# Performance work log

Hardware: AMD Instinct MI355X
Metric: run time of the kernel (lower is better)

The kernel has to match this reference:

```python
import jax, jax.numpy as jnp
import numpy as np

B, S, H = 2, 2048, 2048
NH, HD = 32, 64          # num heads, head dim (H = NH*HD)
ROT = 16                 # rotary_ndims = int(HD * rope_pct=0.25)
THETA = 10000.0
MAXPOS = 4096
NEG_INF = -1e30


def _rope_cache():
    inv_freq = 1.0 / (THETA ** (jnp.arange(0, ROT, 2, dtype=jnp.float32) / ROT))
    t = jnp.arange(MAXPOS, dtype=jnp.float32)
    freqs = jnp.outer(t, inv_freq)              # [MAXPOS, ROT/2]
    emb = jnp.concatenate([freqs, freqs], -1)   # [MAXPOS, ROT]
    return jnp.cos(emb), jnp.sin(emb)


def _rotate_half(x):
    x1, x2 = jnp.split(x, 2, axis=-1)
    return jnp.concatenate([-x2, x1], axis=-1)


def setup_inputs() -> dict:
    key = jax.random.key(0)
    k1, k2, k3 = jax.random.split(key, 3)
    hidden_states = jax.random.normal(k1, (B, S, H), dtype=jnp.float32)
    qkv_w = jax.random.normal(k2, (3 * H, H), dtype=jnp.float32) * 0.02
    o_w = jax.random.normal(k3, (H, H), dtype=jnp.float32) * 0.02
    position_ids = (jnp.arange(B * S).reshape(B, S) % MAXPOS).astype(jnp.int32)
    return {"hidden_states": hidden_states, "qkv_w": qkv_w, "o_w": o_w,
            "position_ids": position_ids}


def reference(hidden_states, qkv_w, o_w, position_ids):
    b, s, _ = hidden_states.shape
    # fused QKV projection (Linear, no bias): x @ W^T
    qkv = hidden_states @ qkv_w.T                      # [b, s, 3H]
    q, k, v = jnp.split(qkv, 3, axis=-1)
    # (b, s, nh*hd) -> (b, nh, s, hd)
    q = q.reshape(b, s, NH, HD).transpose(0, 2, 1, 3)
    k = k.reshape(b, s, NH, HD).transpose(0, 2, 1, 3)
    v = v.reshape(b, s, NH, HD).transpose(0, 2, 1, 3)

    # partial RoPE on first ROT dims
    cos, sin = _rope_cache()
    cos = cos[position_ids][:, None]                   # [b, 1, s, ROT]
    sin = sin[position_ids][:, None]
    q_rot, q_pass = q[..., :ROT], q[..., ROT:]
    k_rot, k_pass = k[..., :ROT], k[..., ROT:]
    q_rot = q_rot * cos + _rotate_half(q_rot) * sin
    k_rot = k_rot * cos + _rotate_half(k_rot) * sin
    q = jnp.concatenate([q_rot, q_pass], axis=-1)
    k = jnp.concatenate([k_rot, k_pass], axis=-1)

    # causal scaled-dot-product attention (prefill branch, layer_past=None)
    scale = 1.0 / jnp.sqrt(jnp.float32(HD))
    scores = jnp.einsum('bhqd,bhkd->bhqk', q, k) * scale
    causal = jnp.tril(jnp.ones((s, s), dtype=bool))
    scores = jnp.where(causal, scores, NEG_INF)
    weights = jax.nn.softmax(scores.astype(jnp.float32), axis=-1).astype(q.dtype)
    attn = jnp.einsum('bhqk,bhkd->bhqd', weights, v)   # [b, nh, s, hd]

    attn = attn.transpose(0, 2, 1, 3).reshape(b, s, NH * HD)
    return attn @ o_w.T
```

## Files before the change

kernel.cpp:

```cpp
#include <hip/hip_runtime.h>
#include <hip/hip_bf16.h>
#include <math.h>

#define B_   2
#define S_   2048
#define H_   2048
#define NH_  32
#define HD_  64

typedef __bf16 bf16_t;
typedef bf16_t bf16x8 __attribute__((ext_vector_type(8)));
typedef float  f32x4  __attribute__((ext_vector_type(4)));
typedef unsigned short u16x8 __attribute__((ext_vector_type(8)));

__device__ __forceinline__ float bf2f(unsigned short u) {
  unsigned int x = ((unsigned int)u) << 16;
  return __builtin_bit_cast(float, x);
}
__device__ __forceinline__ unsigned short f2bf(float f) {
  unsigned int u = __builtin_bit_cast(unsigned int, f);
  u += 0x7FFFu + ((u >> 16) & 1u);
  return (unsigned short)(u >> 16);
}

__device__ __forceinline__ void gload16(const void* g, void* l) {
  __builtin_amdgcn_global_load_lds((const __attribute__((address_space(1))) void*)g,
                                   (__attribute__((address_space(3))) void*)l, 16, 0, 0);
}

__global__ void cast_kernel(const float* __restrict__ in, unsigned short* __restrict__ out, int n4) {
  int stride = gridDim.x * blockDim.x;
  for (int i = blockIdx.x * blockDim.x + threadIdx.x; i < n4; i += stride) {
    float4 v = reinterpret_cast<const float4*>(in)[i];
    ushort4 o;
    o.x = f2bf(v.x); o.y = f2bf(v.y); o.z = f2bf(v.z); o.w = f2bf(v.w);
    reinterpret_cast<ushort4*>(out)[i] = o;
  }
}

template<int EPI>
__global__ __launch_bounds__(256) void gemm_bt(
    const unsigned short* __restrict__ A, const unsigned short* __restrict__ Bt,
    float* __restrict__ outF,
    unsigned short* __restrict__ qb, unsigned short* __restrict__ kb, unsigned short* __restrict__ vb,
    int M, int N, int K)
{
  __shared__ unsigned short As[128 * 64];
  __shared__ unsigned short Bs[128 * 64];
  const int tid  = threadIdx.x;
  const int lane = tid & 63;
  const int wave = tid >> 6;
  const int lo = lane & 15, hi = lane >> 4;
  const int wr = wave >> 1, wc = wave & 1;
  const int m0 = blockIdx.x * 128;
  const int n0 = blockIdx.y * 128;

  const unsigned short* asrc[4];
  const unsigned short* bsrc[4];
  unsigned short* adst[4];
  unsigned short* bdst[4];
#pragma unroll
  for (int i = 0; i < 4; ++i) {
    int idx = i * 256 + tid;
    int r  = idx >> 3;
    int cb = (idx & 7) * 16;
    int cs = cb ^ ((r & 7) << 4);
    asrc[i] = A  + (size_t)(m0 + r) * K + (cs >> 1);
    bsrc[i] = Bt + (size_t)(n0 + r) * K + (cs >> 1);
    adst[i] = &As[idx * 8];
    bdst[i] = &Bs[idx * 8];
  }

  f32x4 zero = {0.f, 0.f, 0.f, 0.f};
  f32x4 acc[4][4];
#pragma unroll
  for (int i = 0; i < 4; ++i)
#pragma unroll
    for (int j = 0; j < 4; ++j) acc[i][j] = zero;

  for (int k0 = 0; k0 < K; k0 += 64) {
    __syncthreads();
#pragma unroll
    for (int i = 0; i < 4; ++i) gload16(asrc[i] + k0, adst[i]);
#pragma unroll
    for (int i = 0; i < 4; ++i) gload16(bsrc[i] + k0, bdst[i]);
    __syncthreads();
#pragma unroll
    for (int kk = 0; kk < 2; ++kk) {
      bf16x8 af[4], bfm[4];
#pragma unroll
      for (int i = 0; i < 4; ++i) {
        int ra = wr * 64 + i * 16 + lo;
        af[i] = *reinterpret_cast<const bf16x8*>(
            (const char*)As + ra * 128 + ((kk * 64 + hi * 16) ^ ((ra & 7) << 4)));
        int rb = wc * 64 + i * 16 + lo;
        bfm[i] = *reinterpret_cast<const bf16x8*>(
            (const char*)Bs + rb * 128 + ((kk * 64 + hi * 16) ^ ((rb & 7) << 4)));
      }
#pragma unroll
      for (int i = 0; i < 4; ++i)
#pragma unroll
        for (int j = 0; j < 4; ++j)
          acc[i][j] = __builtin_amdgcn_mfma_f32_16x16x32_bf16(af[i], bfm[j], acc[i][j], 0, 0, 0);
    }
  }

#pragma unroll
  for (int i = 0; i < 4; ++i) {
#pragma unroll
    for (int j = 0; j < 4; ++j) {
#pragma unroll
      for (int r = 0; r < 4; ++r) {
        int row = m0 + wr * 64 + i * 16 + hi * 4 + r;
        int col = n0 + wc * 64 + j * 16 + lo;
        float v = acc[i][j][r];
        if (EPI == 0) {
          int sec = col >> 11;
          int hh  = (col >> 6) & 31;
          int d   = col & 63;
          int b   = row >> 11;
          int s   = row & 2047;
          unsigned short bv = f2bf(v);
          size_t off = ((size_t)(b * NH_ + hh) * S_ + s) * HD_ + d;
          if (sec == 0)      qb[off] = bv;
          else if (sec == 1) kb[off] = bv;
          else               vb[off] = bv;
        } else {
          outF[(size_t)row * N + col] = v;
        }
      }
    }
  }
}

__global__ __launch_bounds__(256) void vtrans_kernel(const unsigned short* __restrict__ vb,
                                                     unsigned short* __restrict__ vt) {
  __shared__ unsigned short T[64 * 64];
  const int s0 = blockIdx.x * 64;
  const int bh = blockIdx.y;
  const unsigned short* src = vb + (size_t)bh * S_ * HD_ + (size_t)s0 * HD_;
  unsigned short* dst = vt + (size_t)bh * HD_ * S_ + s0;
  const int t = threadIdx.x;
#pragma unroll
  for (int pass = 0; pass < 2; ++pass) {
    int r  = pass * 32 + (t >> 3);
    int c8 = t & 7;
    u16x8 v = *reinterpret_cast<const u16x8*>(src + r * HD_ + c8 * 8);
    *reinterpret_cast<u16x8*>((char*)T + r * 128 + ((c8 * 16) ^ ((r & 7) << 4))) = v;
  }
  __syncthreads();
#pragma unroll
  for (int pass = 0; pass < 2; ++pass) {
    int d  = pass * 32 + (t >> 3);
    int sc = t & 7;
    u16x8 v;
#pragma unroll
    for (int i = 0; i < 8; ++i) {
      int s = sc * 8 + i;
      v[i] = *(const unsigned short*)((const char*)T + s * 128 + ((2 * d) ^ ((s & 7) << 4)));
    }
    *reinterpret_cast<u16x8*>(dst + (size_t)d * S_ + sc * 8) = v;
  }
}

__global__ void rope_kernel(unsigned short* __restrict__ qb, unsigned short* __restrict__ kb,
                            const int* __restrict__ pos) {
  int idx = blockIdx.x * blockDim.x + threadIdx.x;
  if (idx >= B_ * NH_ * S_) return;
  int s  = idx & (S_ - 1);
  int bh = idx >> 11;
  int b  = bh >> 5;
  float p = (float)pos[b * S_ + s];
  const float invf[8] = {1.0f, 0.31622776601683794f, 0.1f, 0.031622776601683791f,
                         0.01f, 0.0031622776601683794f, 0.001f, 0.00031622776601683794f};
  unsigned short* q = qb + (size_t)idx * HD_;
  unsigned short* k = kb + (size_t)idx * HD_;
#pragma unroll
  for (int i = 0; i < 8; ++i) {
    float ang = p * invf[i];
    float sn, c;
    sincosf(ang, &sn, &c);
    float q1 = bf2f(q[i]), q2 = bf2f(q[i + 8]);
    q[i]     = f2bf(q1 * c - q2 * sn);
    q[i + 8] = f2bf(q2 * c + q1 * sn);
    float k1 = bf2f(k[i]), k2 = bf2f(k[i + 8]);
    k[i]     = f2bf(k1 * c - k2 * sn);
    k[i + 8] = f2bf(k2 * c + k1 * sn);
  }
}

__global__ __launch_bounds__(256, 2) void attn_fwd(
    const unsigned short* __restrict__ qb, const unsigned short* __restrict__ kb,
    const unsigned short* __restrict__ vt, unsigned short* __restrict__ ob)
{
  __shared__ unsigned short Ks[2][64 * 64];
  __shared__ unsigned short Vs[2][64 * 64];
  __shared__ unsigned short Ps[4][2][32 * 64];
  const int bid  = blockIdx.x;
  const int j    = bid >> 6;
  const int bh   = bid & 63;
  const int tid  = threadIdx.x;
  const int lane = tid & 63;
  const int wave = tid >> 6;
  const int lo = lane & 15, hi = lane >> 4;
  const int b = bh >> 5, h = bh & 31;
  const unsigned short* Qg = qb + (size_t)bh * S_ * HD_;
  const unsigned short* Kg = kb + (size_t)bh * S_ * HD_;
  const unsigned short* Vg = vt + (size_t)bh * HD_ * S_;

  const int qrow0[2] = {j * 128 + wave * 32, (15 - j) * 128 + wave * 32};

  const float qscale = 0.125f * 1.4426950408889634f;
  bf16x8 aq[2][2][2];
#pragma unroll
  for (int t = 0; t < 2; ++t)
#pragma unroll
    for (int rf = 0; rf < 2; ++rf)
#pragma unroll
      for (int kk = 0; kk < 2; ++kk) {
        bf16x8 tt = *reinterpret_cast<const bf16x8*>(
            Qg + (size_t)(qrow0[t] + rf * 16 + lo) * HD_ + kk * 32 + hi * 8);
#pragma unroll
        for (int e = 0; e < 8; ++e) aq[t][rf][kk][e] = (bf16_t)((float)tt[e] * qscale);
      }

  f32x4 zero = {0.f, 0.f, 0.f, 0.f};
  float m_s[2][2][4], l_s[2][2][4];
  f32x4 o_acc[2][2][4];
#pragma unroll
  for (int t = 0; t < 2; ++t)
#pragma unroll
    for (int rf = 0; rf < 2; ++rf)
#pragma unroll
      for (int r = 0; r < 4; ++r) {
        m_s[t][rf][r] = -1e30f; l_s[t][rf][r] = 0.f;
        o_acc[t][rf][r] = zero;
      }

  auto stage = [&](int kt, int buf) {
#pragma unroll
    for (int i = 0; i < 2; ++i) {
      int idx = i * 256 + tid;
      int r   = idx >> 3;
      int cs  = ((idx & 7) * 16) ^ ((r & 7) << 4);
      gload16(Kg + (size_t)(kt * 64 + r) * HD_ + (cs >> 1), &Ks[buf][idx * 8]);
      gload16(Vg + (size_t)r * S_ + kt * 64 + (cs >> 1), &Vs[buf][idx * 8]);
    }
  };

  const int nkt = 2 * (15 - j) + 2;
  stage(0, 0);

  for (int kt = 0; kt < nkt; ++kt) {
    const int cur = kt & 1;
    if (kt + 1 < nkt) {
      stage(kt + 1, cur ^ 1);
      asm volatile("s_waitcnt vmcnt(4)" ::: "memory");
    } else {
      asm volatile("s_waitcnt vmcnt(0)" ::: "memory");
    }
    __builtin_amdgcn_s_barrier();
    __builtin_amdgcn_sched_barrier(0);

    bf16x8 bk[4][2];
#pragma unroll
    for (int ct = 0; ct < 4; ++ct)
#pragma unroll
      for (int kk = 0; kk < 2; ++kk) {
        int row = ct * 16 + lo;
        bk[ct][kk] = *reinterpret_cast<const bf16x8*>(
            (const char*)&Ks[cur][0] + row * 128 + ((kk * 64 + hi * 16) ^ ((row & 7) << 4)));
      }

#pragma unroll
    for (int t = 0; t < 2; ++t) {
      if (kt * 64 <= qrow0[t] + 31) {
        f32x4 sc[2][4];
        __builtin_amdgcn_s_setprio(1);
#pragma unroll
        for (int rf = 0; rf < 2; ++rf)
#pragma unroll
          for (int ct = 0; ct < 4; ++ct) {
            f32x4 a = zero;
            a = __builtin_amdgcn_mfma_f32_16x16x32_bf16(aq[t][rf][0], bk[ct][0], a, 0, 0, 0);
            a = __builtin_amdgcn_mfma_f32_16x16x32_bf16(aq[t][rf][1], bk[ct][1], a, 0, 0, 0);
            sc[rf][ct] = a;
          }
        __builtin_amdgcn_s_setprio(0);

        if (kt * 64 + 63 > qrow0[t]) {
#pragma unroll
          for (int rf = 0; rf < 2; ++rf)
#pragma unroll
            for (int ct = 0; ct < 4; ++ct)
#pragma unroll
              for (int rr = 0; rr < 4; ++rr) {
                int qrow = qrow0[t] + rf * 16 + hi * 4 + rr;
                int kcol = kt * 64 + ct * 16 + lo;
                if (kcol > qrow) sc[rf][ct][rr] = -1e30f;
              }
        }

#pragma unroll
        for (int rf = 0; rf < 2; ++rf) {
#pragma unroll
          for (int rr = 0; rr < 4; ++rr) {
            float tm = fmaxf(fmaxf(sc[rf][0][rr], sc[rf][1][rr]),
                             fmaxf(sc[rf][2][rr], sc[rf][3][rr]));
            tm = fmaxf(tm, __shfl_xor(tm, 1));
            tm = fmaxf(tm, __shfl_xor(tm, 2));
            tm = fmaxf(tm, __shfl_xor(tm, 4));
            tm = fmaxf(tm, __shfl_xor(tm, 8));
            float mn = fmaxf(m_s[t][rf][rr], tm);
            float corr = exp2f(m_s[t][rf][rr] - mn);
            m_s[t][rf][rr] = mn;
            float rs = 0.f;
#pragma unroll
            for (int ct = 0; ct < 4; ++ct) {
              float e = exp2f(sc[rf][ct][rr] - mn);
              sc[rf][ct][rr] = e;
              rs += e;
            }
            rs += __shfl_xor(rs, 1);
            rs += __shfl_xor(rs, 2);
            rs += __shfl_xor(rs, 4);
            rs += __shfl_xor(rs, 8);
            l_s[t][rf][rr] = l_s[t][rf][rr] * corr + rs;
#pragma unroll
            for (int dt = 0; dt < 4; ++dt) o_acc[t][rf][dt][rr] *= corr;
          }
        }

        char* pw = (char*)&Ps[wave][t][0];
#pragma unroll
        for (int rf = 0; rf < 2; ++rf)
#pragma unroll
          for (int ct = 0; ct < 4; ++ct)
#pragma unroll
            for (int rr = 0; rr < 4; ++rr) {
              int row = rf * 16 + hi * 4 + rr;
              *(unsigned short*)(pw + row * 128 + ((2 * (ct * 16 + lo)) ^ ((row & 7) << 4))) =
                  f2bf(sc[rf][ct][rr]);
            }
      }
    }

    bf16x8 bv[4][2];
#pragma unroll
    for (int dt = 0; dt < 4; ++dt)
#pragma unroll
      for (int kk = 0; kk < 2; ++kk) {
        int row = dt * 16 + lo;
        bv[dt][kk] = *reinterpret_cast<const bf16x8*>(
            (const char*)&Vs[cur][0] + row * 128 + ((kk * 64 + hi * 16) ^ ((row & 7) << 4)));
      }
#pragma unroll
    for (int t = 0; t < 2; ++t) {
      if (kt * 64 <= qrow0[t] + 31) {
        char* pw = (char*)&Ps[wave][t][0];
        bf16x8 ap[2][2];
#pragma unroll
        for (int rf = 0; rf < 2; ++rf)
#pragma unroll
          for (int kk = 0; kk < 2; ++kk) {
            int rowA = rf * 16 + lo;
            ap[rf][kk] = *reinterpret_cast<const bf16x8*>(
                pw + rowA * 128 + ((kk * 64 + hi * 16) ^ ((rowA & 7) << 4)));
          }
        __builtin_amdgcn_s_setprio(1);
#pragma unroll
        for (int rf = 0; rf < 2; ++rf)
#pragma unroll
          for (int dt = 0; dt < 4; ++dt) {
            o_acc[t][rf][dt] = __builtin_amdgcn_mfma_f32_16x16x32_bf16(ap[rf][0], bv[dt][0], o_acc[t][rf][dt], 0, 0, 0);
            o_acc[t][rf][dt] = __builtin_amdgcn_mfma_f32_16x16x32_bf16(ap[rf][1], bv[dt][1], o_acc[t][rf][dt], 0, 0, 0);
          }
        __builtin_amdgcn_s_setprio(0);
      }
    }

    __builtin_amdgcn_s_barrier();
    __builtin_amdgcn_sched_barrier(0);
  }

#pragma unroll
  for (int t = 0; t < 2; ++t)
#pragma unroll
    for (int rf = 0; rf < 2; ++rf) {
      float inv_l[4];
#pragma unroll
      for (int rr = 0; rr < 4; ++rr) inv_l[rr] = 1.f / l_s[t][rf][rr];
#pragma unroll
      for (int dt = 0; dt < 4; ++dt)
#pragma unroll
        for (int rr = 0; rr < 4; ++rr) {
          int srow = qrow0[t] + rf * 16 + hi * 4 + rr;
          int d    = dt * 16 + lo;
          ob[(size_t)(b * S_ + srow) * H_ + h * HD_ + d] = f2bf(o_acc[t][rf][dt][rr] * inv_l[rr]);
        }
    }
}

extern "C" void kernel_launch(void* const* d_in, const int* in_sizes, int n_in,
                              void* d_out, int out_size, void* d_ws, size_t ws_size,
                              hipStream_t stream) {
  (void)in_sizes; (void)n_in; (void)out_size; (void)ws_size;
  const float* hs   = (const float*)d_in[0];
  const float* qkvw = (const float*)d_in[1];
  const float* ow   = (const float*)d_in[2];
  const int*   pos  = (const int*)d_in[3];

  char* ws = (char*)d_ws;
  unsigned short* Xb = (unsigned short*)(ws);
  unsigned short* Wq = (unsigned short*)(ws + (16ull << 20));
  unsigned short* Ob = (unsigned short*)(ws + (40ull << 20));
  unsigned short* Qb = (unsigned short*)(ws + (48ull << 20));
  unsigned short* Kb = (unsigned short*)(ws + (64ull << 20));
  unsigned short* Vb = (unsigned short*)(ws + (80ull << 20));
  unsigned short* Vt = (unsigned short*)(ws + (96ull << 20));

  cast_kernel<<<2048, 256, 0, stream>>>(hs,   Xb, (B_ * S_ * H_) / 4);
  cast_kernel<<<2048, 256, 0, stream>>>(qkvw, Wq, (3 * H_ * H_) / 4);
  cast_kernel<<<2048, 256, 0, stream>>>(ow,   Ob, (H_ * H_) / 4);

  gemm_bt<0><<<dim3(32, 48), 256, 0, stream>>>(Xb, Wq, nullptr, Qb, Kb, Vb,
                                               B_ * S_, 3 * H_, H_);
  vtrans_kernel<<<dim3(S_ / 64, B_ * NH_), 256, 0, stream>>>(Vb, Vt);
  rope_kernel<<<(B_ * NH_ * S_) / 256, 256, 0, stream>>>(Qb, Kb, pos);
  attn_fwd<<<512, 256, 0, stream>>>(Qb, Kb, Vt, Xb);
  gemm_bt<1><<<dim3(32, 16), 256, 0, stream>>>(Xb, Ob, (float*)d_out,
                                               nullptr, nullptr, nullptr,
                                               B_ * S_, H_, H_);
}
```

Measured before the change: 500.1 us.

## Use 256x256 double-buffered 8-wave tile for QKV projection GEMM

Replaces the 128x128 QKV GEMM with a dedicated 256x256-tile kernel using 512 threads, double-buffered LDS staging through global_load_lds, explicit vmcnt waits, and setprio around MFMA bursts. The larger tile raises arithmetic intensity and the double buffering overlaps global loads with compute. The output projection keeps the old kernel, now specialized to the f32 epilogue. The cost is 128 KB of LDS per block, so only one block fits per CU, and the grid drops to 384 blocks, which could leave some CUs idle on a 256-CU part.

```diff
diff --git a/kernel.cpp b/kernel.cpp
--- a/kernel.cpp
+++ b/kernel.cpp
@@ -38,12 +38,116 @@
   }
 }
 
-template<int EPI>
-__global__ __launch_bounds__(256) void gemm_bt(
+__global__ __launch_bounds__(512, 1) void gemm256_qkv(
     const unsigned short* __restrict__ A, const unsigned short* __restrict__ Bt,
-    float* __restrict__ outF,
     unsigned short* __restrict__ qb, unsigned short* __restrict__ kb, unsigned short* __restrict__ vb,
     int M, int N, int K)
+{
+  __shared__ unsigned short As[2][256 * 64];
+  __shared__ unsigned short Bs[2][256 * 64];
+  const int tid  = threadIdx.x;
+  const int lane = tid & 63;
+  const int wave = tid >> 6;
+  const int lo = lane & 15, hi = lane >> 4;
+  const int wr = wave >> 2, wc = wave & 3;
+  const int m0 = blockIdx.x * 256;
+  const int n0 = blockIdx.y * 256;
+
+  auto stage8 = [&](int kt, int buf) {
+#pragma unroll
+    for (int l = 0; l < 4; ++l) {
+      int idx2 = l * 512 + tid;
+      int r  = idx2 >> 3;
+      int cs = ((idx2 & 7) * 16) ^ ((r & 7) << 4);
+      gload16(A  + (size_t)(m0 + r) * K + kt * 64 + (cs >> 1), &As[buf][idx2 * 8]);
+      gload16(Bt + (size_t)(n0 + r) * K + kt * 64 + (cs >> 1), &Bs[buf][idx2 * 8]);
+    }
+  };
+
+  f32x4 zero = {0.f, 0.f, 0.f, 0.f};
+  f32x4 acc[8][4];
+#pragma unroll
+  for (int i = 0; i < 8; ++i)
+#pragma unroll
+    for (int j = 0; j < 4; ++j) acc[i][j] = zero;
+
+  stage8(0, 0);
+  const int NK = K / 64;
+  for (int j = 0; j < NK; ++j) {
+    const int P = j & 1;
+    if (j + 1 < NK) {
+      stage8(j + 1, P ^ 1);
+      asm volatile("s_waitcnt vmcnt(8)" ::: "memory");
+    } else {
+      asm volatile("s_waitcnt vmcnt(0)" ::: "memory");
+    }
+    __builtin_amdgcn_s_barrier();
+
+    bf16x8 bfr[4][2];
+#pragma unroll
+    for (int nf = 0; nf < 4; ++nf)
+#pragma unroll
+      for (int kk = 0; kk < 2; ++kk) {
+        int rb = wc * 64 + nf * 16 + lo;
+        bfr[nf][kk] = *reinterpret_cast<const bf16x8*>(
+            (const char*)&Bs[P][0] + rb * 128 + ((kk * 64 + hi * 16) ^ ((rb & 7) << 4)));
+      }
+
+#pragma unroll
+    for (int p = 0; p < 4; ++p) {
+      bf16x8 afr[2][2];
+#pragma unroll
+      for (int m2 = 0; m2 < 2; ++m2)
+#pragma unroll
+        for (int kk = 0; kk < 2; ++kk) {
+          int ra = wr * 128 + (p * 2 + m2) * 16 + lo;
+          afr[m2][kk] = *reinterpret_cast<const bf16x8*>(
+              (const char*)&As[P][0] + ra * 128 + ((kk * 64 + hi * 16) ^ ((ra & 7) << 4)));
+        }
+      __builtin_amdgcn_s_barrier();
+      asm volatile("s_waitcnt lgkmcnt(0)" ::: "memory");
+      __builtin_amdgcn_sched_barrier(0);
+      __builtin_amdgcn_s_setprio(1);
+#pragma unroll
+      for (int m2 = 0; m2 < 2; ++m2)
+#pragma unroll
+        for (int nf = 0; nf < 4; ++nf) {
+          acc[p * 2 + m2][nf] = __builtin_amdgcn_mfma_f32_16x16x32_bf16(
+              afr[m2][0], bfr[nf][0], acc[p * 2 + m2][nf], 0, 0, 0);
+          acc[p * 2 + m2][nf] = __builtin_amdgcn_mfma_f32_16x16x32_bf16(
+              afr[m2][1], bfr[nf][1], acc[p * 2 + m2][nf], 0, 0, 0);
+        }
+      __builtin_amdgcn_s_setprio(0);
+      __builtin_amdgcn_s_barrier();
+    }
+  }
+
+#pragma unroll
+  for (int mf = 0; mf < 8; ++mf) {
+#pragma unroll
+    for (int nf = 0; nf < 4; ++nf) {
+#pragma unroll
+      for (int rr = 0; rr < 4; ++rr) {
+        int row = m0 + wr * 128 + mf * 16 + hi * 4 + rr;
+        int col = n0 + wc * 64 + nf * 16 + lo;
+        int sec = col >> 11;
+        int hh  = (col >> 6) & 31;
+        int d   = col & 63;
+        int b   = row >> 11;
+        int s   = row & 2047;
+        unsigned short bv = f2bf(acc[mf][nf][rr]);
+        size_t off = ((size_t)(b * NH_ + hh) * S_ + s) * HD_ + d;
+        if (sec == 0)      qb[off] = bv;
+        else if (sec == 1) kb[off] = bv;
+        else               vb[off] = bv;
+      }
+    }
+  }
+}
+
+__global__ __launch_bounds__(256) void gemm_bt_f32(
+    const unsigned short* __restrict__ A, const unsigned short* __restrict__ Bt,
+    float* __restrict__ outF, int M, int N, int K)
 {
   __shared__ unsigned short As[128 * 64];
   __shared__ unsigned short Bs[128 * 64];
@@ -106,31 +210,15 @@
   }
 
 #pragma unroll
-  for (int i = 0; i < 4; ++i) {
-#pragma unroll
-    for (int j = 0; j < 4; ++j) {
+  for (int i = 0; i < 4; ++i)
+#pragma unroll
+    for (int j = 0; j < 4; ++j)
 #pragma unroll
       for (int r = 0; r < 4; ++r) {
         int row = m0 + wr * 64 + i * 16 + hi * 4 + r;
         int col = n0 + wc * 64 + j * 16 + lo;
-        float v = acc[i][j][r];
-        if (EPI == 0) {
-          int sec = col >> 11;
-          int hh  = (col >> 6) & 31;
-          int d   = col & 63;
-          int b   = row >> 11;
-          int s   = row & 2047;
-          unsigned short bv = f2bf(v);
-          size_t off = ((size_t)(b * NH_ + hh) * S_ + s) * HD_ + d;
-          if (sec == 0)      qb[off] = bv;
-          else if (sec == 1) kb[off] = bv;
-          else               vb[off] = bv;
-        } else {
-          outF[(size_t)row * N + col] = v;
-        }
-      }
-    }
-  }
+        outF[(size_t)row * N + col] = acc[i][j][r];
+      }
 }
 
 __global__ __launch_bounds__(256) void vtrans_kernel(const unsigned short* __restrict__ vb,
@@ -423,12 +511,11 @@
   cast_kernel<<<2048, 256, 0, stream>>>(qkvw, Wq, (3 * H_ * H_) / 4);
   cast_kernel<<<2048, 256, 0, stream>>>(ow,   Ob, (H_ * H_) / 4);
 
-  gemm_bt<0><<<dim3(32, 48), 256, 0, stream>>>(Xb, Wq, nullptr, Qb, Kb, Vb,
-                                               B_ * S_, 3 * H_, H_);
+  gemm256_qkv<<<dim3(16, 24), 512, 0, stream>>>(Xb, Wq, Qb, Kb, Vb,
+                                                B_ * S_, 3 * H_, H_);
   vtrans_kernel<<<dim3(S_ / 64, B_ * NH_), 256, 0, stream>>>(Vb, Vt);
   rope_kernel<<<(B_ * NH_ * S_) / 256, 256, 0, stream>>>(Qb, Kb, pos);
   attn_fwd<<<512, 256, 0, stream>>>(Qb, Kb, Vt, Xb);
-  gemm_bt<1><<<dim3(32, 16), 256, 0, stream>>>(Xb, Ob, (float*)d_out,
-                                               nullptr, nullptr, nullptr,
-                                               B_ * S_, H_, H_);
-}
+  gemm_bt_f32<<<dim3(32, 16), 256, 0, stream>>>(Xb, Ob, (float*)d_out,
+                                                B_ * S_, H_, H_);
+}
```

Measured after the change: 532.8 us. 1.07x slower.
